# Kernel tuning notes

Hardware: AMD Instinct MI355X
Metric: run time of the kernel (lower is better)

Reference implementation:

```python
import jax, jax.numpy as jnp
import numpy as np

N, E, F, H, C, ED = 10000, 160000, 4, 32, 4, 2  # nodes, edges, in_feat, hidden, classes, edge_dim


def _init(key, shape, fan_in):
    return jax.random.normal(key, shape, jnp.float32) / np.float32(np.sqrt(fan_in))


def setup_inputs() -> dict:
    key = jax.random.key(0)
    ks = iter(jax.random.split(key, 40))
    inp = {
        "x": jax.random.normal(next(ks), (N, F), jnp.float32),
        "edge_index": jax.random.randint(next(ks), (2, E), 0, N, dtype=jnp.int32),
        "edge_attr": jax.random.normal(next(ks), (E, ED), jnp.float32),
    }
    for i, din in enumerate([F, H, H]):
        inp[f"w1_{i}"] = _init(next(ks), (ED, H), ED)
        inp[f"b1_{i}"] = jnp.zeros((H,), jnp.float32)
        inp[f"w2_{i}"] = _init(next(ks), (H, din * H), H)
        inp[f"b2_{i}"] = jnp.zeros((din * H,), jnp.float32)
        inp[f"root_{i}"] = _init(next(ks), (din, H), din)
        inp[f"bias_{i}"] = jnp.zeros((H,), jnp.float32)
    inp["fc_w"] = _init(next(ks), (H, C), H)
    inp["fc_b"] = jnp.zeros((C,), jnp.float32)
    return inp


def _nnconv(x, src, dst, edge_attr, w1, b1, w2, b2, root, bias):
    # edge MLP -> per-edge weight matrix [E, din, H]
    h = jax.nn.relu(edge_attr @ w1 + b1)                      # [E, H]
    W = (h @ w2 + b2).reshape(E, x.shape[1], -1)              # [E, din, H]
    msg = jnp.einsum('ei,eio->eo', x[src], W)                 # gather + per-edge matvec
    agg = jax.ops.segment_sum(msg, dst, num_segments=N)       # scatter-add to targets
    return agg + x @ root + bias                              # root weight + bias (NNConv)


def reference(x, edge_index, edge_attr,
              w1_0, b1_0, w2_0, b2_0, root_0, bias_0,
              w1_1, b1_1, w2_1, b2_1, root_1, bias_1,
              w1_2, b1_2, w2_2, b2_2, root_2, bias_2,
              fc_w, fc_b):
    src, dst = edge_index[0], edge_index[1]
    layers = [(w1_0, b1_0, w2_0, b2_0, root_0, bias_0),
              (w1_1, b1_1, w2_1, b2_1, root_1, bias_1),
              (w1_2, b1_2, w2_2, b2_2, root_2, bias_2)]
    for p in layers:
        x = jax.nn.relu(_nnconv(x, src, dst, edge_attr, *p))  # dropout=0 -> no-op
    logits = x @ fc_w + fc_b
    return jax.nn.log_softmax(logits, axis=1)
```

## Files before the change

### kernel.cpp

```cpp
#include <hip/hip_runtime.h>
#include <hip/hip_bf16.h>
#include <math.h>

#define N_NODES 10000
#define N_EDGES 160000

typedef __attribute__((ext_vector_type(8))) short bf16x8;
typedef __attribute__((ext_vector_type(4))) float f32x4;

static __device__ inline unsigned short f2b(float v) {
    __hip_bfloat16 b = __float2bfloat16(v);
    return *reinterpret_cast<unsigned short*>(&b);
}

__global__ __launch_bounds__(256) void k_tw2z(const float* __restrict__ s0,
                                              const float* __restrict__ s1,
                                              const float* __restrict__ s2,
                                              float* __restrict__ t0,
                                              float* __restrict__ t1,
                                              float* __restrict__ t2,
                                              int* __restrict__ cnt) {
    int tid = blockIdx.x * 256 + threadIdx.x;
    if (tid < 10240) { cnt[tid] = 0; return; }
    int d = tid - 10240;
    if (d < 4096) {
        int i = d >> 10, j = d & 1023, o = j >> 5, k = j & 31;
        t0[d] = s0[k * 128 + i * 32 + o];
    } else if (d < 4096 + 32768) {
        int q = d - 4096;
        int i = q >> 10, j = q & 1023, o = j >> 5, k = j & 31;
        t1[q] = s1[k * 1024 + i * 32 + o];
    } else if (d < 4096 + 65536) {
        int q = d - 4096 - 32768;
        int i = q >> 10, j = q & 1023, o = j >> 5, k = j & 31;
        t2[q] = s2[k * 1024 + i * 32 + o];
    }
}

__global__ __launch_bounds__(256) void k_hist(const int* __restrict__ ei,
                                              int* __restrict__ cnt) {
    int e = blockIdx.x * 256 + threadIdx.x;
    if (e < N_EDGES) atomicAdd(&cnt[ei[e]], 1);
}

__global__ __launch_bounds__(256) void k_scan(const int* __restrict__ cnt,
                                              int* __restrict__ off,
                                              int* __restrict__ cursor) {
    __shared__ int part[256];
    int t = threadIdx.x;
    int base = t * 40;
    int s = 0;
    for (int i = 0; i < 40; ++i) {
        int idx = base + i;
        if (idx < N_NODES) s += cnt[idx];
    }
    part[t] = s;
    __syncthreads();
    for (int d = 1; d < 256; d <<= 1) {
        int v = (t >= d) ? part[t - d] : 0;
        __syncthreads();
        part[t] += v;
        __syncthreads();
    }
    int run = part[t] - s;
    for (int i = 0; i < 40; ++i) {
        int idx = base + i;
        if (idx < N_NODES) {
            off[idx] = run;
            cursor[idx] = run;
            run += cnt[idx];
        }
    }
    if (t == 255) off[N_NODES] = run;
}

__global__ __launch_bounds__(256) void k_scatter_h(const int* __restrict__ ei,
                                                   const float* __restrict__ ea,
                                                   int* __restrict__ cursor,
                                                   int* __restrict__ dst_s,
                                                   const float* __restrict__ w1a, const float* __restrict__ b1a,
                                                   const float* __restrict__ w1b, const float* __restrict__ b1b,
                                                   const float* __restrict__ w1c, const float* __restrict__ b1c,
                                                   unsigned short* __restrict__ h0,
                                                   unsigned short* __restrict__ h1,
                                                   unsigned short* __restrict__ h2) {
    int e = blockIdx.x * 256 + threadIdx.x;
    if (e >= N_EDGES) return;
    float a0 = ea[2 * e], a1 = ea[2 * e + 1];
    int src = ei[e], dst = ei[N_EDGES + e];
    int pos = atomicAdd(&cursor[src], 1);
    dst_s[pos] = dst;
    const float* W1[3] = {w1a, w1b, w1c};
    const float* B1[3] = {b1a, b1b, b1c};
    unsigned short* H[3] = {h0, h1, h2};
#pragma unroll
    for (int l = 0; l < 3; ++l) {
        unsigned int pk[16];
#pragma unroll
        for (int j = 0; j < 16; ++j) {
            float v0 = fmaxf(a0 * W1[l][2 * j]     + a1 * W1[l][32 + 2 * j]     + B1[l][2 * j],     0.f);
            float v1 = fmaxf(a0 * W1[l][2 * j + 1] + a1 * W1[l][32 + 2 * j + 1] + B1[l][2 * j + 1], 0.f);
            pk[j] = (unsigned int)f2b(v0) | ((unsigned int)f2b(v1) << 16);
        }
        uint4* dp = (uint4*)(H[l] + (size_t)pos * 32);
        dp[0] = make_uint4(pk[0], pk[1], pk[2], pk[3]);
        dp[1] = make_uint4(pk[4], pk[5], pk[6], pk[7]);
        dp[2] = make_uint4(pk[8], pk[9], pk[10], pk[11]);
        dp[3] = make_uint4(pk[12], pk[13], pk[14], pk[15]);
    }
}

template <int DIN, bool FIRST>
__global__ __launch_bounds__(256) void k_G(const float* __restrict__ xin,
                                           const float* __restrict__ w2t,
                                           const float* __restrict__ b2,
                                           const float* __restrict__ root,
                                           const float* __restrict__ bias,
                                           unsigned short* __restrict__ Gb,
                                           float* __restrict__ xb2,
                                           float* __restrict__ agg) {
    const int t = threadIdx.x;
    const int n0 = blockIdx.x * 16;

    __shared__ float xs[16 * DIN];
    for (int idx = t; idx < 16 * DIN; idx += 256) {
        int m = idx / DIN, i = idx - m * DIN;
        float v = xin[(size_t)(n0 + m) * DIN + i];
        if (!FIRST) v = v > 0.f ? v : 0.f;
        xs[idx] = v;
    }
    __syncthreads();

    float acc[16][4];
#pragma unroll
    for (int m = 0; m < 16; ++m)
        acc[m][0] = acc[m][1] = acc[m][2] = acc[m][3] = 0.f;

#pragma unroll
    for (int i = 0; i < DIN; ++i) {
        const float4 w = *(const float4*)(w2t + i * 1024 + t * 4);
#pragma unroll
        for (int m = 0; m < 16; ++m) {
            float xv = xs[m * DIN + i];
            acc[m][0] += xv * w.x;
            acc[m][1] += xv * w.y;
            acc[m][2] += xv * w.z;
            acc[m][3] += xv * w.w;
        }
    }
#pragma unroll
    for (int m = 0; m < 16; ++m) {
        unsigned int p0 = (unsigned int)f2b(acc[m][0]) | ((unsigned int)f2b(acc[m][1]) << 16);
        unsigned int p1 = (unsigned int)f2b(acc[m][2]) | ((unsigned int)f2b(acc[m][3]) << 16);
        *(uint2*)(Gb + (size_t)(n0 + m) * 1024 + t * 4) = make_uint2(p0, p1);
    }

    for (int idx = t; idx < 512; idx += 256) {
        int m = idx >> 5, o = idx & 31;
        float ab = 0.f, ar = bias[o];
#pragma unroll
        for (int i = 0; i < DIN; ++i) {
            float xv = xs[m * DIN + i];
            ab += xv * b2[i * 32 + o];
            ar += xv * root[i * 32 + o];
        }
        size_t p = (size_t)(n0 + m) * 32 + o;
        xb2[p] = ab;
        agg[p] = ar;
    }
}

__global__ __launch_bounds__(256) void k_edge(const int* __restrict__ off,
                                              const int* __restrict__ dst_s,
                                              const unsigned short* __restrict__ hb,
                                              const unsigned short* __restrict__ Gb,
                                              const float* __restrict__ xb2,
                                              float* __restrict__ agg) {
    int t = threadIdx.x;
    int lane = t & 63;
    int n = blockIdx.x * 4 + (t >> 6);
    int col = lane & 15;
    int quad = lane >> 4;

    const bf16x8 b_lo = *(const bf16x8*)(Gb + (size_t)n * 1024 + col * 32 + quad * 8);
    const bf16x8 b_hi = *(const bf16x8*)(Gb + (size_t)n * 1024 + (col + 16) * 32 + quad * 8);
    float xb_lo = xb2[(size_t)n * 32 + col];
    float xb_hi = xb2[(size_t)n * 32 + 16 + col];

    int jb = off[n], je = off[n + 1];
    for (int e0 = jb; e0 < je; e0 += 16) {
        int eA = e0 + col;
        bf16x8 afrag = {0, 0, 0, 0, 0, 0, 0, 0};
        if (eA < je) afrag = *(const bf16x8*)(hb + (size_t)eA * 32 + quad * 8);
        f32x4 acc_lo = {xb_lo, xb_lo, xb_lo, xb_lo};
        f32x4 acc_hi = {xb_hi, xb_hi, xb_hi, xb_hi};
        acc_lo = __builtin_amdgcn_mfma_f32_16x16x32_bf16(afrag, b_lo, acc_lo, 0, 0, 0);
        acc_hi = __builtin_amdgcn_mfma_f32_16x16x32_bf16(afrag, b_hi, acc_hi, 0, 0, 0);
#pragma unroll
        for (int r = 0; r < 4; ++r) {
            int er = e0 + quad * 4 + r;
            if (er < je) {
                int d = dst_s[er];
                atomicAdd(&agg[(size_t)d * 32 + col], acc_lo[r]);
                atomicAdd(&agg[(size_t)d * 32 + 16 + col], acc_hi[r]);
            }
        }
    }
}

__global__ __launch_bounds__(64) void k_final(const float* __restrict__ agg,
                                              const float* __restrict__ fcw,
                                              const float* __restrict__ fcb,
                                              float* __restrict__ out) {
    int n = blockIdx.x * 64 + threadIdx.x;
    if (n >= N_NODES) return;
    float l0 = fcb[0], l1 = fcb[1], l2 = fcb[2], l3 = fcb[3];
#pragma unroll
    for (int o = 0; o < 32; ++o) {
        float xv = agg[(size_t)n * 32 + o];
        xv = xv > 0.f ? xv : 0.f;
        l0 += xv * fcw[o * 4 + 0];
        l1 += xv * fcw[o * 4 + 1];
        l2 += xv * fcw[o * 4 + 2];
        l3 += xv * fcw[o * 4 + 3];
    }
    float m = fmaxf(fmaxf(l0, l1), fmaxf(l2, l3));
    float s = expf(l0 - m) + expf(l1 - m) + expf(l2 - m) + expf(l3 - m);
    float lse = m + logf(s);
    out[(size_t)n * 4 + 0] = l0 - lse;
    out[(size_t)n * 4 + 1] = l1 - lse;
    out[(size_t)n * 4 + 2] = l2 - lse;
    out[(size_t)n * 4 + 3] = l3 - lse;
}

extern "C" void kernel_launch(void* const* d_in, const int* in_sizes, int n_in,
                              void* d_out, int out_size, void* d_ws, size_t ws_size,
                              hipStream_t stream) {
    const float* x0 = (const float*)d_in[0];
    const int*   ei = (const int*)d_in[1];
    const float* ea = (const float*)d_in[2];
    const float *W1[3], *B1[3], *W2[3], *B2[3], *RT[3], *BS[3];
    for (int l = 0; l < 3; ++l) {
        W1[l] = (const float*)d_in[3 + 6 * l];
        B1[l] = (const float*)d_in[4 + 6 * l];
        W2[l] = (const float*)d_in[5 + 6 * l];
        B2[l] = (const float*)d_in[6 + 6 * l];
        RT[l] = (const float*)d_in[7 + 6 * l];
        BS[l] = (const float*)d_in[8 + 6 * l];
    }
    const float* fcw = (const float*)d_in[21];
    const float* fcb = (const float*)d_in[22];
    float* out = (float*)d_out;

    int*   cnt    = (int*)d_ws;
    int*   cursor = cnt + 10240;
    int*   off    = cursor + 10240;
    int*   dst_s  = off + 10240;
    float* w2t0   = (float*)(dst_s + 160000);
    float* w2t1   = w2t0 + 4096;
    float* w2t2   = w2t1 + 32768;
    float* xb2    = w2t2 + 32768;
    float* aggA   = xb2 + 320000;
    float* aggB   = aggA + 320000;
    unsigned short* h0 = (unsigned short*)(aggB + 320000);
    unsigned short* h1 = h0 + 5120000;
    unsigned short* h2 = h1 + 5120000;
    unsigned short* Gb = h2 + 5120000;

    const int gE256 = (N_EDGES + 255) / 256;
    const int gG    = N_NODES / 16;
    const int gEdge = N_NODES / 4;

    k_tw2z<<<312, 256, 0, stream>>>(W2[0], W2[1], W2[2], w2t0, w2t1, w2t2, cnt);
    k_hist<<<gE256, 256, 0, stream>>>(ei, cnt);
    k_scan<<<1, 256, 0, stream>>>(cnt, off, cursor);
    k_scatter_h<<<gE256, 256, 0, stream>>>(ei, ea, cursor, dst_s,
                                           W1[0], B1[0], W1[1], B1[1], W1[2], B1[2],
                                           h0, h1, h2);

    k_G<4, true><<<gG, 256, 0, stream>>>(x0, w2t0, B2[0], RT[0], BS[0], Gb, xb2, aggA);
    k_edge<<<gEdge, 256, 0, stream>>>(off, dst_s, h0, Gb, xb2, aggA);

    k_G<32, false><<<gG, 256, 0, stream>>>(aggA, w2t1, B2[1], RT[1], BS[1], Gb, xb2, aggB);
    k_edge<<<gEdge, 256, 0, stream>>>(off, dst_s, h1, Gb, xb2, aggB);

    k_G<32, false><<<gG, 256, 0, stream>>>(aggB, w2t2, B2[2], RT[2], BS[2], Gb, xb2, aggA);
    k_edge<<<gEdge, 256, 0, stream>>>(off, dst_s, h2, Gb, xb2, aggA);

    k_final<<<(N_NODES + 63) / 64, 64, 0, stream>>>(aggA, fcw, fcb, out);
}
```

Baseline: 278.8 us.

## Replace atomic scatter-add with dst-sorted message buffer and segmented reduction

Builds a second CSR keyed by destination and a permutation mapping each src-sorted edge to its dst-sorted slot. Each edge kernel now writes its 32-float message to a dense buffer at that slot, and a new aggregation kernel sums each destination's contiguous messages without atomics. This removes the float atomics into agg, which are contended and nondeterministic. In exchange it adds a 20 MB message buffer write and read per layer, three extra kernel launches, and a second histogram and scan.

```diff
diff --git a/kernel.cpp b/kernel.cpp
--- a/kernel.cpp
+++ b/kernel.cpp
@@ -19,10 +19,10 @@
                                               float* __restrict__ t0,
                                               float* __restrict__ t1,
                                               float* __restrict__ t2,
-                                              int* __restrict__ cnt) {
+                                              int* __restrict__ cnt2) {
     int tid = blockIdx.x * 256 + threadIdx.x;
-    if (tid < 10240) { cnt[tid] = 0; return; }
-    int d = tid - 10240;
+    if (tid < 20480) { cnt2[tid] = 0; return; }
+    int d = tid - 20480;
     if (d < 4096) {
         int i = d >> 10, j = d & 1023, o = j >> 5, k = j & 31;
         t0[d] = s0[k * 128 + i * 32 + o];
@@ -38,14 +38,23 @@
 }
 
 __global__ __launch_bounds__(256) void k_hist(const int* __restrict__ ei,
-                                              int* __restrict__ cnt) {
+                                              int* __restrict__ cnt_src,
+                                              int* __restrict__ cnt_dst) {
     int e = blockIdx.x * 256 + threadIdx.x;
-    if (e < N_EDGES) atomicAdd(&cnt[ei[e]], 1);
-}
-
-__global__ __launch_bounds__(256) void k_scan(const int* __restrict__ cnt,
-                                              int* __restrict__ off,
-                                              int* __restrict__ cursor) {
+    if (e >= N_EDGES) return;
+    atomicAdd(&cnt_src[ei[e]], 1);
+    atomicAdd(&cnt_dst[ei[N_EDGES + e]], 1);
+}
+
+__global__ __launch_bounds__(256) void k_scan(const int* __restrict__ cnt_src,
+                                              const int* __restrict__ cnt_dst,
+                                              int* __restrict__ off_src,
+                                              int* __restrict__ off_dst,
+                                              int* __restrict__ cur_src,
+                                              int* __restrict__ cur_dst) {
+    const int* cnt = blockIdx.x == 0 ? cnt_src : cnt_dst;
+    int* off = blockIdx.x == 0 ? off_src : off_dst;
+    int* cur = blockIdx.x == 0 ? cur_src : cur_dst;
     __shared__ int part[256];
     int t = threadIdx.x;
     int base = t * 40;
@@ -67,7 +76,7 @@
         int idx = base + i;
         if (idx < N_NODES) {
             off[idx] = run;
-            cursor[idx] = run;
+            cur[idx] = run;
             run += cnt[idx];
         }
     }
@@ -76,8 +85,9 @@
 
 __global__ __launch_bounds__(256) void k_scatter_h(const int* __restrict__ ei,
                                                    const float* __restrict__ ea,
-                                                   int* __restrict__ cursor,
-                                                   int* __restrict__ dst_s,
+                                                   int* __restrict__ cur_src,
+                                                   int* __restrict__ cur_dst,
+                                                   int* __restrict__ perm,
                                                    const float* __restrict__ w1a, const float* __restrict__ b1a,
                                                    const float* __restrict__ w1b, const float* __restrict__ b1b,
                                                    const float* __restrict__ w1c, const float* __restrict__ b1c,
@@ -88,8 +98,8 @@
     if (e >= N_EDGES) return;
     float a0 = ea[2 * e], a1 = ea[2 * e + 1];
     int src = ei[e], dst = ei[N_EDGES + e];
-    int pos = atomicAdd(&cursor[src], 1);
-    dst_s[pos] = dst;
+    int pos = atomicAdd(&cur_src[src], 1);
+    perm[pos] = atomicAdd(&cur_dst[dst], 1);
     const float* W1[3] = {w1a, w1b, w1c};
     const float* B1[3] = {b1a, b1b, b1c};
     unsigned short* H[3] = {h0, h1, h2};
@@ -170,12 +180,12 @@
     }
 }
 
-__global__ __launch_bounds__(256) void k_edge(const int* __restrict__ off,
-                                              const int* __restrict__ dst_s,
+__global__ __launch_bounds__(256) void k_edge(const int* __restrict__ off_src,
+                                              const int* __restrict__ perm,
                                               const unsigned short* __restrict__ hb,
                                               const unsigned short* __restrict__ Gb,
                                               const float* __restrict__ xb2,
-                                              float* __restrict__ agg) {
+                                              float* __restrict__ msgf) {
     int t = threadIdx.x;
     int lane = t & 63;
     int n = blockIdx.x * 4 + (t >> 6);
@@ -187,7 +197,7 @@
     float xb_lo = xb2[(size_t)n * 32 + col];
     float xb_hi = xb2[(size_t)n * 32 + 16 + col];
 
-    int jb = off[n], je = off[n + 1];
+    int jb = off_src[n], je = off_src[n + 1];
     for (int e0 = jb; e0 < je; e0 += 16) {
         int eA = e0 + col;
         bf16x8 afrag = {0, 0, 0, 0, 0, 0, 0, 0};
@@ -200,12 +210,25 @@
         for (int r = 0; r < 4; ++r) {
             int er = e0 + quad * 4 + r;
             if (er < je) {
-                int d = dst_s[er];
-                atomicAdd(&agg[(size_t)d * 32 + col], acc_lo[r]);
-                atomicAdd(&agg[(size_t)d * 32 + 16 + col], acc_hi[r]);
+                size_t p = (size_t)perm[er] * 32;
+                msgf[p + col] = acc_lo[r];
+                msgf[p + 16 + col] = acc_hi[r];
             }
         }
     }
+}
+
+__global__ __launch_bounds__(256) void k_agg(const int* __restrict__ off_dst,
+                                             const float* __restrict__ msgf,
+                                             float* __restrict__ agg) {
+    int t = threadIdx.x;
+    int n = blockIdx.x * 8 + (t >> 5);
+    int o = t & 31;
+    int jb = off_dst[n], je = off_dst[n + 1];
+    float s = 0.f;
+    for (int j = jb; j < je; ++j)
+        s += msgf[(size_t)j * 32 + o];
+    agg[(size_t)n * 32 + o] += s;
 }
 
 __global__ __launch_bounds__(64) void k_final(const float* __restrict__ agg,
@@ -252,17 +275,21 @@
     const float* fcb = (const float*)d_in[22];
     float* out = (float*)d_out;
 
-    int*   cnt    = (int*)d_ws;
-    int*   cursor = cnt + 10240;
-    int*   off    = cursor + 10240;
-    int*   dst_s  = off + 10240;
-    float* w2t0   = (float*)(dst_s + 160000);
-    float* w2t1   = w2t0 + 4096;
-    float* w2t2   = w2t1 + 32768;
-    float* xb2    = w2t2 + 32768;
-    float* aggA   = xb2 + 320000;
-    float* aggB   = aggA + 320000;
-    unsigned short* h0 = (unsigned short*)(aggB + 320000);
+    int*   cnt_src = (int*)d_ws;
+    int*   cnt_dst = cnt_src + 10240;
+    int*   cur_src = cnt_dst + 10240;
+    int*   cur_dst = cur_src + 10240;
+    int*   off_src = cur_dst + 10240;
+    int*   off_dst = off_src + 10240;
+    int*   perm    = off_dst + 10240;
+    float* w2t0    = (float*)(perm + 163840);
+    float* w2t1    = w2t0 + 4096;
+    float* w2t2    = w2t1 + 32768;
+    float* xb2     = w2t2 + 32768;
+    float* aggA    = xb2 + 320000;
+    float* aggB    = aggA + 320000;
+    float* msgf    = aggB + 320000;
+    unsigned short* h0 = (unsigned short*)(msgf + 5120000);
     unsigned short* h1 = h0 + 5120000;
     unsigned short* h2 = h1 + 5120000;
     unsigned short* Gb = h2 + 5120000;
@@ -270,22 +297,26 @@
     const int gE256 = (N_EDGES + 255) / 256;
     const int gG    = N_NODES / 16;
     const int gEdge = N_NODES / 4;
-
-    k_tw2z<<<312, 256, 0, stream>>>(W2[0], W2[1], W2[2], w2t0, w2t1, w2t2, cnt);
-    k_hist<<<gE256, 256, 0, stream>>>(ei, cnt);
-    k_scan<<<1, 256, 0, stream>>>(cnt, off, cursor);
-    k_scatter_h<<<gE256, 256, 0, stream>>>(ei, ea, cursor, dst_s,
+    const int gAgg  = N_NODES / 8;
+
+    k_tw2z<<<352, 256, 0, stream>>>(W2[0], W2[1], W2[2], w2t0, w2t1, w2t2, cnt_src);
+    k_hist<<<gE256, 256, 0, stream>>>(ei, cnt_src, cnt_dst);
+    k_scan<<<2, 256, 0, stream>>>(cnt_src, cnt_dst, off_src, off_dst, cur_src, cur_dst);
+    k_scatter_h<<<gE256, 256, 0, stream>>>(ei, ea, cur_src, cur_dst, perm,
                                            W1[0], B1[0], W1[1], B1[1], W1[2], B1[2],
                                            h0, h1, h2);
 
     k_G<4, true><<<gG, 256, 0, stream>>>(x0, w2t0, B2[0], RT[0], BS[0], Gb, xb2, aggA);
-    k_edge<<<gEdge, 256, 0, stream>>>(off, dst_s, h0, Gb, xb2, aggA);
+    k_edge<<<gEdge, 256, 0, stream>>>(off_src, perm, h0, Gb, xb2, msgf);
+    k_agg<<<gAgg, 256, 0, stream>>>(off_dst, msgf, aggA);
 
     k_G<32, false><<<gG, 256, 0, stream>>>(aggA, w2t1, B2[1], RT[1], BS[1], Gb, xb2, aggB);
-    k_edge<<<gEdge, 256, 0, stream>>>(off, dst_s, h1, Gb, xb2, aggB);
+    k_edge<<<gEdge, 256, 0, stream>>>(off_src, perm, h1, Gb, xb2, msgf);
+    k_agg<<<gAgg, 256, 0, stream>>>(off_dst, msgf, aggB);
 
     k_G<32, false><<<gG, 256, 0, stream>>>(aggB, w2t2, B2[2], RT[2], BS[2], Gb, xb2, aggA);
-    k_edge<<<gEdge, 256, 0, stream>>>(off, dst_s, h2, Gb, xb2, aggA);
+    k_edge<<<gEdge, 256, 0, stream>>>(off_src, perm, h2, Gb, xb2, msgf);
+    k_agg<<<gAgg, 256, 0, stream>>>(off_dst, msgf, aggA);
 
     k_final<<<(N_NODES + 63) / 64, 64, 0, stream>>>(aggA, fcw, fcb, out);
 }
```

Measured after the change: 285.5 us. 1.02x slower.
